# Kernel tuning notes

Measured on AMD Instinct MI355X. Metric: run time of the kernel, lower is better.

Reference implementation:

```python
import jax, jax.numpy as jnp
import numpy as np

D_MODEL = 1024
D_KV = 64
N_HEADS = 16
KV_HEADS = 4
G = N_HEADS // KV_HEADS
NUM_BUCKETS = 32
MAX_DISTANCE = 128


def _relative_position_bucket(relative_position, bidirectional=True,
                              num_buckets=NUM_BUCKETS, max_distance=MAX_DISTANCE):
    # Faithful port of T5Attention._relative_position_bucket
    relative_buckets = jnp.zeros_like(relative_position)
    if bidirectional:
        num_buckets //= 2
        relative_buckets = (relative_position > 0).astype(jnp.int32) * num_buckets
        relative_position = jnp.abs(relative_position)
    else:
        relative_position = -jnp.minimum(relative_position, 0)
    max_exact = num_buckets // 2
    is_small = relative_position < max_exact
    rel_if_large = max_exact + (
        jnp.log(relative_position.astype(jnp.float32) / max_exact)
        / np.log(max_distance / max_exact) * (num_buckets - max_exact)
    ).astype(jnp.int32)
    rel_if_large = jnp.minimum(rel_if_large, num_buckets - 1)
    return relative_buckets + jnp.where(is_small, relative_position, rel_if_large)


def setup_inputs() -> dict:
    key = jax.random.key(0)
    ks = jax.random.split(key, 6)
    B, S = 2, 2048
    inner = N_HEADS * D_KV
    sc = 1.0 / np.sqrt(D_MODEL)
    return {
        "hidden_states": jax.random.normal(ks[0], (B, S, D_MODEL), dtype=jnp.float32),
        "Wq": jax.random.normal(ks[1], (D_MODEL, inner), dtype=jnp.float32) * sc,
        "Wk": jax.random.normal(ks[2], (D_MODEL, inner), dtype=jnp.float32) * sc,
        "Wv": jax.random.normal(ks[3], (D_MODEL, inner), dtype=jnp.float32) * sc,
        "Wo": jax.random.normal(ks[4], (inner, D_MODEL), dtype=jnp.float32) * sc,
        "rel_bias": jax.random.normal(ks[5], (NUM_BUCKETS, N_HEADS), dtype=jnp.float32) * 0.1,
    }


def reference(hidden_states, Wq, Wk, Wv, Wo, rel_bias):
    B, S, _ = hidden_states.shape

    def split_heads(x):  # [B,S,inner] -> [B,H,S,Dk]
        return x.reshape(B, S, N_HEADS, D_KV).transpose(0, 2, 1, 3)

    q = split_heads(hidden_states @ Wq)
    k = split_heads(hidden_states @ Wk)
    v = split_heads(hidden_states @ Wv)

    # head index = g * KV_HEADS + h (einops 'b (g h) ...' with h=kv_heads)
    gq = q.reshape(B, G, KV_HEADS, S, D_KV)
    gk = k.reshape(B, G, KV_HEADS, S, D_KV).mean(axis=1)  # [B,Hkv,S,Dk]
    # einsum sums over g (as in torch.einsum 'bghnd,bhsd->bhns'); no 1/sqrt(d) in T5
    scores = jnp.einsum('bghnd,bhsd->bhns', gq, gk)  # [B,Hkv,S,S]

    # T5 relative position bias (bidirectional, encoder)
    ctx = jnp.arange(S)[:, None]
    mem = jnp.arange(S)[None, :]
    buckets = _relative_position_bucket(mem - ctx, bidirectional=True)
    bias = rel_bias[buckets]                # [S,S,H]
    bias = bias.transpose(2, 0, 1)[None]    # [1,H,S,S]
    gbias = bias.reshape(1, G, KV_HEADS, S, S).mean(axis=1)  # [1,Hkv,S,S]

    scores = scores + gbias
    attn = jax.nn.softmax(scores.astype(jnp.float32), axis=-1).astype(scores.dtype)

    # repeat grouped attn weights back to full heads: 'b h n s -> b (g h) n s'
    attn_full = jnp.tile(attn, (1, G, 1, 1))  # [B,H,S,S]
    ctx_out = jnp.einsum('bhns,bhsd->bhnd', attn_full, v)  # [B,H,S,Dk]
    ctx_out = ctx_out.transpose(0, 2, 1, 3).reshape(B, S, N_HEADS * D_KV)
    return ctx_out @ Wo  # [B,S,D_MODEL]
```

## Files before the change

kernel.cpp:

```cpp
#include <hip/hip_runtime.h>
#include <math.h>


typedef __bf16 bf16_t;
typedef bf16_t bf16x8 __attribute__((ext_vector_type(8)));
typedef bf16_t bf16x4 __attribute__((ext_vector_type(4)));
typedef float f32x4 __attribute__((ext_vector_type(4)));

#define MFMA16(a, b, c) __builtin_amdgcn_mfma_f32_16x16x32_bf16(a, b, c, 0, 0, 0)

typedef __attribute__((address_space(1))) void gvoid;
typedef __attribute__((address_space(3))) void svoid;
__device__ __forceinline__ void gld16(const void* g, void* l) {
    __builtin_amdgcn_global_load_lds((gvoid*)g, (svoid*)l, 16, 0, 0);
}

__global__ __launch_bounds__(256) void prep_all(const float* __restrict__ hs,
                                                const float* __restrict__ Wq,
                                                const float* __restrict__ Wk,
                                                const float* __restrict__ Wv,
                                                const float* __restrict__ Wo,
                                                const float* __restrict__ rel_bias,
                                                bf16_t* __restrict__ hs_hi,
                                                bf16_t* __restrict__ hs_lo,
                                                bf16_t* __restrict__ Thi,
                                                bf16_t* __restrict__ Tlo,
                                                bf16_t* __restrict__ WvT,
                                                bf16_t* __restrict__ WoT,
                                                float* __restrict__ btab) {
    __shared__ float sm[2048];
    const int r = blockIdx.x, t = threadIdx.x;
    if (r < 4096) {
        size_t idx = ((size_t)r * 256 + t) * 4;
        float4 v = *(const float4*)(hs + idx);
        bf16x4 h, l;
        h[0] = (bf16_t)v.x; l[0] = (bf16_t)(v.x - (float)h[0]);
        h[1] = (bf16_t)v.y; l[1] = (bf16_t)(v.y - (float)h[1]);
        h[2] = (bf16_t)v.z; l[2] = (bf16_t)(v.z - (float)h[2]);
        h[3] = (bf16_t)v.w; l[3] = (bf16_t)(v.w - (float)h[3]);
        *(bf16x4*)(hs_hi + idx) = h;
        *(bf16x4*)(hs_lo + idx) = l;
    } else if (r < 5120) {
        int k = r - 4096;
        float* rq = sm;
        float* rk = sm + 1024;
#pragma unroll
        for (int j = 0; j < 4; ++j) {
            rq[t + j * 256] = Wq[(size_t)k * 1024 + t + j * 256];
            rk[t + j * 256] = Wk[(size_t)k * 1024 + t + j * 256];
        }
        __syncthreads();
        int h = t >> 6, j2 = t & 63;
        float sq = 0.f, sk = 0.f;
#pragma unroll
        for (int g = 0; g < 4; ++g) {
            sq += rq[(g * 4 + h) * 64 + j2];
            sk += rk[(g * 4 + h) * 64 + j2];
        }
        sk *= 0.25f;
        bf16_t qh = (bf16_t)sq;
        Thi[(size_t)t * 1024 + k] = qh;
        Tlo[(size_t)t * 1024 + k] = (bf16_t)(sq - (float)qh);
        bf16_t kh = (bf16_t)sk;
        Thi[(size_t)(256 + t) * 1024 + k] = kh;
        Tlo[(size_t)(256 + t) * 1024 + k] = (bf16_t)(sk - (float)kh);
    } else if (r < 7168) {
        const float* src = (r < 6144) ? Wv : Wo;
        bf16_t* dst = (r < 6144) ? WvT : WoT;
        int rr = (r < 6144) ? r - 5120 : r - 6144;
        int bx = (rr & 31) * 32, by = (rr >> 5) * 32;
        int tx = t & 31, ty = t >> 5;
        float(*tile)[33] = (float(*)[33])sm;
#pragma unroll
        for (int i = 0; i < 32; i += 8)
            tile[ty + i][tx] = src[(size_t)(by + ty + i) * 1024 + bx + tx];
        __syncthreads();
#pragma unroll
        for (int i = 0; i < 32; i += 8)
            dst[(size_t)(bx + ty + i) * 1024 + by + tx] = (bf16_t)tile[tx][ty + i];
    } else {
        int idx = (r - 7168) * 256 + t;
        if (idx >= 4095) return;
        int delta = idx - 2047;
        int bucket = (delta > 0) ? 16 : 0;
        int arp = delta < 0 ? -delta : delta;
        int rb;
        if (arp < 8) {
            rb = arp;
        } else {
            float tt = (logf((float)arp * 0.125f) / 2.772588722239781f) * 8.0f;
            int ri = 8 + (int)tt;
            rb = ri < 15 ? ri : 15;
        }
        bucket += rb;
#pragma unroll
        for (int h = 0; h < 4; ++h) {
            float s = 0.25f * (rel_bias[bucket * 16 + h] + rel_bias[bucket * 16 + h + 4] +
                               rel_bias[bucket * 16 + h + 8] + rel_bias[bucket * 16 + h + 12]);
            btab[h * 4608 + idx] = s;
        }
    }
}

__global__ __launch_bounds__(256, 1) void proj_qkv(const bf16_t* __restrict__ Ah,
                                                   const bf16_t* __restrict__ Al,
                                                   const bf16_t* __restrict__ Bh,
                                                   const bf16_t* __restrict__ Bl,
                                                   const bf16_t* __restrict__ WvT,
                                                   bf16_t* __restrict__ Qhi,
                                                   bf16_t* __restrict__ Qlo,
                                                   bf16_t* __restrict__ Kbh,
                                                   bf16_t* __restrict__ Kbl,
                                                   bf16_t* __restrict__ Vb) {
    __shared__ bf16_t pool[36864];
    const int K = 1024, nk = 32;
    const int t = threadIdx.x;
    const int w = t >> 6, lane = t & 63;
    const int lr = lane & 15, q = lane >> 4;
    const int l = blockIdx.y * 16 + blockIdx.x;
    const int nl = (l & 7) * 64 + (l >> 3);
    const int bx = nl & 15;
    const int m0 = (nl >> 4) * 128;
    const bool qk = bx < 8;
    const int n0 = qk ? bx * 64 : (bx - 8) * 128;
    const int mw = (w & 1) * 64;
    f32x4 acc[4][4] = {};

    const int rA = t & 127, cA0 = t >> 7, cA1 = 2 + (t >> 7);
    const size_t oA0 = (size_t)(m0 + rA) * K + cA0 * 8;
    const size_t oA1 = (size_t)(m0 + rA) * K + cA1 * 8;
    const int rBq = t & 63, cBq = t >> 6;
    const size_t oBq = (size_t)(n0 + rBq) * K + cBq * 8;
    const size_t oBv0 = (size_t)(n0 + rA) * K + cA0 * 8;
    const size_t oBv1 = (size_t)(n0 + rA) * K + cA1 * 8;

    auto stage = [&](int bf, int kidx) {
        bf16_t* base = &pool[bf * 12288];
        const int k0 = kidx * 32;
        gld16(Ah + oA0 + k0, base + t * 8);
        gld16(Ah + oA1 + k0, base + (256 + t) * 8);
        if (qk) {
            gld16(Al + oA0 + k0, base + 4096 + t * 8);
            gld16(Al + oA1 + k0, base + 4096 + (256 + t) * 8);
            gld16(Bh + oBq + k0, base + 8192 + t * 8);
            gld16(Bl + oBq + k0, base + 10240 + t * 8);
        } else {
            gld16(WvT + oBv0 + k0, base + 4096 + t * 8);
            gld16(WvT + oBv1 + k0, base + 4096 + (256 + t) * 8);
        }
    };

    stage(0, 0);
    stage(1, 1);
    stage(2, 2);
    if (qk)
        asm volatile("s_waitcnt vmcnt(12)" ::: "memory");
    else
        asm volatile("s_waitcnt vmcnt(8)" ::: "memory");
    __builtin_amdgcn_s_barrier();

    int cur = 0;
    for (int it = 0; it < nk; ++it) {
        const bf16_t* base = &pool[cur * 12288];
        if (qk) {
            const int nw = (w >> 1) * 32;
            bf16x8 ah[4], al[4], bh[2], bl[2];
#pragma unroll
            for (int i = 0; i < 4; ++i) {
                int sa = (q * 128 + mw + i * 16 + lr) * 8;
                ah[i] = *(const bf16x8*)&base[sa];
                al[i] = *(const bf16x8*)&base[4096 + sa];
            }
#pragma unroll
            for (int j = 0; j < 2; ++j) {
                int sb = (q * 64 + nw + j * 16 + lr) * 8;
                bh[j] = *(const bf16x8*)&base[8192 + sb];
                bl[j] = *(const bf16x8*)&base[10240 + sb];
            }
            asm volatile("s_waitcnt lgkmcnt(0)" ::: "memory");
            if (it < nk - 2)
                asm volatile("s_waitcnt vmcnt(6)" ::: "memory");
            else
                asm volatile("s_waitcnt vmcnt(0)" ::: "memory");
            __builtin_amdgcn_s_barrier();
            if (it + 3 < nk) stage(cur, it + 3);
#pragma unroll
            for (int i = 0; i < 4; ++i)
#pragma unroll
                for (int j = 0; j < 2; ++j) {
                    acc[i][j] = MFMA16(ah[i], bh[j], acc[i][j]);
                    acc[i][j] = MFMA16(ah[i], bl[j], acc[i][j]);
                    acc[i][j] = MFMA16(al[i], bh[j], acc[i][j]);
                }
        } else {
            const int nw = (w >> 1) * 64;
            bf16x8 af[4], bfv[4];
#pragma unroll
            for (int i = 0; i < 4; ++i)
                af[i] = *(const bf16x8*)&base[(q * 128 + mw + i * 16 + lr) * 8];
#pragma unroll
            for (int j = 0; j < 4; ++j)
                bfv[j] = *(const bf16x8*)&base[4096 + (q * 128 + nw + j * 16 + lr) * 8];
            asm volatile("s_waitcnt lgkmcnt(0)" ::: "memory");
            if (it < nk - 2)
                asm volatile("s_waitcnt vmcnt(4)" ::: "memory");
            else
                asm volatile("s_waitcnt vmcnt(0)" ::: "memory");
            __builtin_amdgcn_s_barrier();
            if (it + 3 < nk) stage(cur, it + 3);
#pragma unroll
            for (int i = 0; i < 4; ++i)
#pragma unroll
                for (int j = 0; j < 4; ++j) acc[i][j] = MFMA16(af[i], bfv[j], acc[i][j]);
        }
        cur = (cur == 2) ? 0 : cur + 1;
    }

    if (qk) {
        const int nwq = (w >> 1) * 32;
#pragma unroll
        for (int i = 0; i < 4; ++i) {
            int row = m0 + mw + i * 16 + q * 4;
#pragma unroll
            for (int j = 0; j < 2; ++j) {
                int col = n0 + nwq + j * 16 + lr;
#pragma unroll
                for (int reg = 0; reg < 4; ++reg) {
                    float x = acc[i][j][reg];
                    int token = row + reg;
                    bf16_t hi = (bf16_t)x;
                    bf16_t lo = (bf16_t)(x - (float)hi);
                    if (col < 256) {
                        size_t o = (size_t)token * 256 + col;
                        Qhi[o] = hi;
                        Qlo[o] = lo;
                    } else {
                        int hc = col - 256;
                        int hh = hc >> 6, d = hc & 63;
                        int b = token >> 11, s = token & 2047;
                        int it2 = s >> 6, sl = s & 63;
                        size_t o = ((size_t)((b * 4 + hh) * 32 + it2)) * 4096 +
                                   (size_t)((d >> 3) * 64 + sl) * 8 + (d & 7);
                        Kbh[o] = hi;
                        Kbl[o] = lo;
                    }
                }
            }
        }
    } else {
        const int nwq = (w >> 1) * 64;
#pragma unroll
        for (int i = 0; i < 4; ++i) {
            int row = m0 + mw + i * 16 + q * 4;
            int b = row >> 11, s = row & 2047;
            int it2 = s >> 6, sc2 = (s >> 3) & 7, si = s & 7;
#pragma unroll
            for (int j = 0; j < 4; ++j) {
                int col = n0 + nwq + j * 16 + lr;
                int hh = (col >> 6) & 3, g = col >> 8, d = col & 63;
                size_t o = ((size_t)((b * 4 + hh) * 32 + it2)) * 16384 +
                           (size_t)(sc2 * 256 + g * 64 + d) * 8 + si;
                bf16x4 pv;
#pragma unroll
                for (int reg = 0; reg < 4; ++reg) pv[reg] = (bf16_t)acc[i][j][reg];
                *(bf16x4*)(Vb + o) = pv;
            }
        }
    }
}

__global__ __launch_bounds__(256, 1) void gemm_out(const bf16_t* __restrict__ A,
                                                   const bf16_t* __restrict__ BT,
                                                   float* __restrict__ C,
                                                   int M, int N, int K) {
    __shared__ bf16_t pool[18432];
    const int t = threadIdx.x;
    const int w = t >> 6, lane = t & 63;
    const int lr = lane & 15, q = lane >> 4;
    const int l = blockIdx.y * 16 + blockIdx.x;
    const int nl = (l & 7) * 64 + (l >> 3);
    const int m0 = (nl >> 4) * 128, n0 = (nl & 15) * 64;
    const int mw = (w & 1) * 64, nw = (w >> 1) * 32;
    f32x4 acc[4][2] = {};
    const int nk = K >> 5;

    const int rA = t & 127, cA0 = t >> 7, cA1 = 2 + (t >> 7);
    const bf16_t* gA0 = A + (size_t)(m0 + rA) * K + cA0 * 8;
    const bf16_t* gA1 = A + (size_t)(m0 + rA) * K + cA1 * 8;
    const bf16_t* gB = BT + (size_t)(n0 + (t & 63)) * K + (t >> 6) * 8;

    auto stage = [&](int bf, int kidx) {
        bf16_t* base = &pool[bf * 6144];
        const int k0 = kidx * 32;
        gld16(gA0 + k0, base + t * 8);
        gld16(gA1 + k0, base + (256 + t) * 8);
        gld16(gB + k0, base + 4096 + t * 8);
    };

    stage(0, 0);
    stage(1, 1);
    stage(2, 2);
    asm volatile("s_waitcnt vmcnt(6)" ::: "memory");
    __builtin_amdgcn_s_barrier();

    int cur = 0;
    for (int it = 0; it < nk; ++it) {
        const bf16_t* base = &pool[cur * 6144];
        bf16x8 af[4], bfv[2];
#pragma unroll
        for (int i = 0; i < 4; ++i)
            af[i] = *(const bf16x8*)&base[(q * 128 + mw + i * 16 + lr) * 8];
#pragma unroll
        for (int j = 0; j < 2; ++j)
            bfv[j] = *(const bf16x8*)&base[4096 + (q * 64 + nw + j * 16 + lr) * 8];
        asm volatile("s_waitcnt lgkmcnt(0)" ::: "memory");
        if (it < nk - 2)
            asm volatile("s_waitcnt vmcnt(3)" ::: "memory");
        else
            asm volatile("s_waitcnt vmcnt(0)" ::: "memory");
        __builtin_amdgcn_s_barrier();
        if (it + 3 < nk) stage(cur, it + 3);
#pragma unroll
        for (int i = 0; i < 4; ++i)
#pragma unroll
            for (int j = 0; j < 2; ++j) acc[i][j] = MFMA16(af[i], bfv[j], acc[i][j]);
        cur = (cur == 2) ? 0 : cur + 1;
    }

#pragma unroll
    for (int i = 0; i < 4; ++i) {
        int row = m0 + mw + i * 16 + q * 4;
#pragma unroll
        for (int j = 0; j < 2; ++j) {
            int col = n0 + nw + j * 16 + lr;
#pragma unroll
            for (int reg = 0; reg < 4; ++reg)
                C[(size_t)(row + reg) * N + col] = acc[i][j][reg];
        }
    }
}

__global__ __launch_bounds__(512, 1) void attn_mfma(const bf16_t* __restrict__ Qhi,
                                                    const bf16_t* __restrict__ Qlo,
                                                    const bf16_t* __restrict__ Kbh,
                                                    const bf16_t* __restrict__ Kbl,
                                                    const bf16_t* __restrict__ Vb,
                                                    const float* __restrict__ btab,
                                                    bf16_t* __restrict__ part0,
                                                    bf16_t* __restrict__ part1,
                                                    float* __restrict__ Sml) {
    __shared__ bf16_t Kh[2][4096], Kl[2][4096], Vsm[2][16384], Ps[8192];
    const int t = threadIdx.x, w = t >> 6, lane = t & 63;
    const int lr = lane & 15, q = lane >> 4;
    const int bl0 = blockIdx.x;
    const int blk = (bl0 & 7) * 32 + (bl0 >> 3);
    const int half = blk & 1, qt = (blk >> 1) & 15, h = (blk >> 5) & 3, b = blk >> 7;
    const int n0 = qt * 128;
    const int rowbase = n0 + w * 16;
    const int swz = (lr & 7) << 3;
    const int psb = w * 1024 + lr * 64;

    const size_t qrow = (size_t)(b * 2048 + rowbase + lr) * 256 + h * 64;
    bf16x8 aqh[2], aql[2];
#pragma unroll
    for (int kb = 0; kb < 2; ++kb) {
        aqh[kb] = *(const bf16x8*)(Qhi + qrow + kb * 32 + q * 8);
        aql[kb] = *(const bf16x8*)(Qlo + qrow + kb * 32 + q * 8);
    }

    const int tilebase = (b * 4 + h) * 32 + half * 16;
    const bf16_t* gK = Kbh + (size_t)tilebase * 4096;
    const bf16_t* gL = Kbl + (size_t)tilebase * 4096;
    const bf16_t* gV = Vb + (size_t)tilebase * 16384;
    const float* btabh = btab + h * 4608 + 2047;

    auto stage = [&](int bf, int it) {
        gld16(gK + (size_t)it * 4096 + t * 8, &Kh[bf][t * 8]);
        gld16(gL + (size_t)it * 4096 + t * 8, &Kl[bf][t * 8]);
        const bf16_t* v0 = gV + (size_t)it * 16384;
#pragma unroll
        for (int j = 0; j < 4; ++j)
            gld16(v0 + (j * 512 + t) * 8, &Vsm[bf][(j * 512 + t) * 8]);
    };

    float m_r = -INFINITY, l_r = 0.f;
    f32x4 O[16] = {};

    stage(0, 0);
    __syncthreads();
    for (int it = 0; it < 16; ++it) {
        const int cur = it & 1;
        if (it + 1 < 16) stage(cur ^ 1, it + 1);
        const int s0g = half * 1024 + it * 64;

        f32x4 sc[4];
#pragma unroll
        for (int ct = 0; ct < 4; ++ct) {
            f32x4 z = {0.f, 0.f, 0.f, 0.f};
#pragma unroll
            for (int kb = 0; kb < 2; ++kb) {
                int sb = ((kb * 4 + q) * 64 + ct * 16 + lr) * 8;
                bf16x8 bh = *(const bf16x8*)&Kh[cur][sb];
                bf16x8 bl = *(const bf16x8*)&Kl[cur][sb];
                z = MFMA16(bh, aqh[kb], z);
                z = MFMA16(bh, aql[kb], z);
                z = MFMA16(bl, aqh[kb], z);
            }
            sc[ct] = z;
        }
        const int dbase = (s0g + q * 4) - (rowbase + lr);
#pragma unroll
        for (int ct = 0; ct < 4; ++ct)
#pragma unroll
            for (int reg = 0; reg < 4; ++reg)
                sc[ct][reg] += btabh[dbase + ct * 16 + reg];

        float mt = fmaxf(fmaxf(sc[0][0], sc[0][1]), fmaxf(sc[0][2], sc[0][3]));
#pragma unroll
        for (int ct = 1; ct < 4; ++ct)
            mt = fmaxf(mt, fmaxf(fmaxf(sc[ct][0], sc[ct][1]), fmaxf(sc[ct][2], sc[ct][3])));
        mt = fmaxf(mt, __shfl_xor(mt, 16, 64));
        mt = fmaxf(mt, __shfl_xor(mt, 32, 64));

        float mn = fmaxf(m_r, mt);
        float al = __expf(m_r - mn);
        m_r = mn;
        float rs = 0.f;
#pragma unroll
        for (int ct = 0; ct < 4; ++ct) {
            bf16x4 tq;
#pragma unroll
            for (int reg = 0; reg < 4; ++reg) {
                float p = __expf(sc[ct][reg] - mn);
                rs += p;
                tq[reg] = (bf16_t)p;
            }
            *(bf16x4*)&Ps[psb + ((ct * 16 + q * 4) ^ swz)] = tq;
        }
        rs += __shfl_xor(rs, 16, 64);
        rs += __shfl_xor(rs, 32, 64);
        l_r = l_r * al + rs;

        bf16x8 pf0 = *(const bf16x8*)&Ps[psb + ((q * 8) ^ swz)];
        bf16x8 pf1 = *(const bf16x8*)&Ps[psb + ((32 + q * 8) ^ swz)];

#pragma unroll
        for (int nt = 0; nt < 16; ++nt) {
            f32x4 o = O[nt];
#pragma unroll
            for (int reg = 0; reg < 4; ++reg) o[reg] *= al;
            bf16x8 v0 = *(const bf16x8*)&Vsm[cur][(q * 256 + nt * 16 + lr) * 8];
            o = MFMA16(v0, pf0, o);
            bf16x8 v1 = *(const bf16x8*)&Vsm[cur][((4 + q) * 256 + nt * 16 + lr) * 8];
            o = MFMA16(v1, pf1, o);
            O[nt] = o;
        }
        __syncthreads();
    }

    bf16_t* P = half ? part1 : part0;
    const float inv = 1.f / l_r;
    const int tokb = b * 2048 + rowbase;
#pragma unroll
    for (int G = 0; G < 4; ++G) {
#pragma unroll
        for (int g4 = 0; g4 < 4; ++g4) {
            int nt = G * 4 + g4;
            bf16x4 tq;
#pragma unroll
            for (int reg = 0; reg < 4; ++reg) tq[reg] = (bf16_t)(O[nt][reg] * inv);
            *(bf16x4*)&Ps[psb + ((g4 * 16 + q * 4) ^ swz)] = tq;
        }
#pragma unroll
        for (int i = 0; i < 2; ++i) {
            int row = i * 8 + (lane >> 3), cv = (lane & 7) * 8;
            bf16x8 fr = *(const bf16x8*)&Ps[w * 1024 + row * 64 + (cv ^ ((row & 7) << 3))];
            *(bf16x8*)(P + (size_t)(tokb + row) * 1024 + (G * 4 + h) * 64 + cv) = fr;
        }
    }
    if (lane < 16)
        Sml[half * 16384 + (size_t)(tokb + lane) * 4 + h] = m_r + logf(l_r);
}

__global__ __launch_bounds__(256) void combine_halves(bf16_t* __restrict__ p0,
                                                      const bf16_t* __restrict__ p1,
                                                      const float* __restrict__ Sml) {
    size_t flat = ((size_t)blockIdx.x * 256 + threadIdx.x) * 8;
    int tok = (int)(flat >> 10), c = (int)(flat & 1023), h = (c >> 6) & 3;
    float s0 = Sml[tok * 4 + h], s1 = Sml[16384 + tok * 4 + h];
    float M = fmaxf(s0, s1);
    float e0 = __expf(s0 - M), e1 = __expf(s1 - M);
    float r = 1.f / (e0 + e1);
    float w0 = e0 * r, w1 = e1 * r;
    bf16x8 a = *(bf16x8*)(p0 + flat);
    bf16x8 bb = *(const bf16x8*)(p1 + flat);
    bf16x8 o;
#pragma unroll
    for (int i = 0; i < 8; ++i) o[i] = (bf16_t)(w0 * (float)a[i] + w1 * (float)bb[i]);
    *(bf16x8*)(p0 + flat) = o;
}

extern "C" void kernel_launch(void* const* d_in, const int* in_sizes, int n_in,
                              void* d_out, int out_size, void* d_ws, size_t ws_size,
                              hipStream_t stream) {
    const float* hs = (const float*)d_in[0];
    const float* Wq = (const float*)d_in[1];
    const float* Wk = (const float*)d_in[2];
    const float* Wv = (const float*)d_in[3];
    const float* Wo = (const float*)d_in[4];
    const float* rb = (const float*)d_in[5];
    float* out = (float*)d_out;

    const size_t MB = 1 << 20;
    const size_t KB = 1 << 10;
    char* ws = (char*)d_ws;
    bf16_t* hs_hi = (bf16_t*)(ws);
    bf16_t* hs_lo = (bf16_t*)(ws + 8 * MB);
    bf16_t* WqkThi = (bf16_t*)(ws + 16 * MB);
    bf16_t* WqkTlo = (bf16_t*)(ws + 17 * MB);
    bf16_t* WvT = (bf16_t*)(ws + 18 * MB);
    bf16_t* WoT = (bf16_t*)(ws + 20 * MB);
    float* btab = (float*)(ws + 22 * MB);
    float* Sml = (float*)(ws + 22 * MB + 128 * KB);
    bf16_t* Qhi = (bf16_t*)(ws + 22 * MB + 256 * KB);
    bf16_t* Qlo = Qhi + (size_t)4096 * 256;
    bf16_t* Kbh = Qlo + (size_t)4096 * 256;
    bf16_t* Kbl = Kbh + (size_t)4096 * 256;
    bf16_t* Vb = Kbl + (size_t)4096 * 256;
    bf16_t* part0 = hs_hi;
    bf16_t* part1 = hs_lo;

    prep_all<<<7184, 256, 0, stream>>>(hs, Wq, Wk, Wv, Wo, rb, hs_hi, hs_lo, WqkThi,
                                       WqkTlo, WvT, WoT, btab);
    proj_qkv<<<dim3(16, 32), 256, 0, stream>>>(hs_hi, hs_lo, WqkThi, WqkTlo, WvT, Qhi,
                                               Qlo, Kbh, Kbl, Vb);
    attn_mfma<<<256, 512, 0, stream>>>(Qhi, Qlo, Kbh, Kbl, Vb, btab, part0, part1, Sml);
    combine_halves<<<2048, 256, 0, stream>>>(part0, part1, Sml);
    gemm_out<<<dim3(16, 32), 256, 0, stream>>>(part0, WoT, out, 4096, 1024, 1024);
}
```

Measured before the change: 220.9 us.

## Fuse split-KV combine into output GEMM and skip redundant attention work

Removes the separate combine_halves kernel by having gemm_out load both partial attention outputs, weight them with the log-sum-exp factors, and write the merged bf16 tile into shared memory before the MFMA loop. The A-operand staging moves from async global-to-LDS copies with triple buffering to register loads plus LDS writes with double buffering. The attention kernel also adds a constant relative-bias value for tiles far from the diagonal, where every bucket saturates, and skips rescaling the O accumulator when no row maximum changed. The costs are a shallower GEMM pipeline, extra ALU work in the GEMM, and more branching in the attention loop.

Result: slower. 232.2 us (+5.1%).

```diff
diff --git a/kernel.cpp b/kernel.cpp
--- a/kernel.cpp
+++ b/kernel.cpp
@@ -269,11 +269,13 @@
     }
 }
 
-__global__ __launch_bounds__(256, 1) void gemm_out(const bf16_t* __restrict__ A,
+__global__ __launch_bounds__(256, 1) void gemm_out(const bf16_t* __restrict__ p0,
+                                                   const bf16_t* __restrict__ p1,
+                                                   const float* __restrict__ Sml,
                                                    const bf16_t* __restrict__ BT,
-                                                   float* __restrict__ C,
-                                                   int M, int N, int K) {
-    __shared__ bf16_t pool[18432];
+                                                   float* __restrict__ C) {
+    __shared__ bf16_t pool[12288];
+    const int K = 1024, N = 1024;
     const int t = threadIdx.x;
     const int w = t >> 6, lane = t & 63;
     const int lr = lane & 15, q = lane >> 4;
@@ -282,49 +284,88 @@
     const int m0 = (nl >> 4) * 128, n0 = (nl & 15) * 64;
     const int mw = (w & 1) * 64, nw = (w >> 1) * 32;
     f32x4 acc[4][2] = {};
-    const int nk = K >> 5;
-
-    const int rA = t & 127, cA0 = t >> 7, cA1 = 2 + (t >> 7);
-    const bf16_t* gA0 = A + (size_t)(m0 + rA) * K + cA0 * 8;
-    const bf16_t* gA1 = A + (size_t)(m0 + rA) * K + cA1 * 8;
+
+    const int rA = t & 127, cA0 = t >> 7;
+    const int tok = m0 + rA;
+    const bf16_t* gA0 = p0 + (size_t)tok * K + cA0 * 8;
+    const bf16_t* gA1 = p1 + (size_t)tok * K + cA0 * 8;
     const bf16_t* gB = BT + (size_t)(n0 + (t & 63)) * K + (t >> 6) * 8;
 
-    auto stage = [&](int bf, int kidx) {
-        bf16_t* base = &pool[bf * 6144];
+    float w00, w01, w02, w03, w10, w11, w12, w13;
+    {
+        float s0, s1, M_, e0, e1, r;
+#define MKW(H, W0, W1)                                   \
+    s0 = Sml[tok * 4 + H];                               \
+    s1 = Sml[16384 + tok * 4 + H];                       \
+    M_ = fmaxf(s0, s1);                                  \
+    e0 = __expf(s0 - M_);                                \
+    e1 = __expf(s1 - M_);                                \
+    r = 1.f / (e0 + e1);                                 \
+    W0 = e0 * r;                                         \
+    W1 = e1 * r;
+        MKW(0, w00, w10)
+        MKW(1, w01, w11)
+        MKW(2, w02, w12)
+        MKW(3, w03, w13)
+#undef MKW
+    }
+
+    bf16x8 sa0, sb0, sa1, sb1;
+    auto stage_load = [&](int kidx) {
         const int k0 = kidx * 32;
-        gld16(gA0 + k0, base + t * 8);
-        gld16(gA1 + k0, base + (256 + t) * 8);
-        gld16(gB + k0, base + 4096 + t * 8);
+        sa0 = *(const bf16x8*)(gA0 + k0);
+        sb0 = *(const bf16x8*)(gA1 + k0);
+        sa1 = *(const bf16x8*)(gA0 + k0 + 16);
+        sb1 = *(const bf16x8*)(gA1 + k0 + 16);
     };
-
-    stage(0, 0);
-    stage(1, 1);
-    stage(2, 2);
-    asm volatile("s_waitcnt vmcnt(6)" ::: "memory");
-    __builtin_amdgcn_s_barrier();
-
-    int cur = 0;
-    for (int it = 0; it < nk; ++it) {
-        const bf16_t* base = &pool[cur * 6144];
-        bf16x8 af[4], bfv[2];
-#pragma unroll
-        for (int i = 0; i < 4; ++i)
-            af[i] = *(const bf16x8*)&base[(q * 128 + mw + i * 16 + lr) * 8];
-#pragma unroll
-        for (int j = 0; j < 2; ++j)
-            bfv[j] = *(const bf16x8*)&base[4096 + (q * 64 + nw + j * 16 + lr) * 8];
-        asm volatile("s_waitcnt lgkmcnt(0)" ::: "memory");
-        if (it < nk - 2)
-            asm volatile("s_waitcnt vmcnt(3)" ::: "memory");
-        else
-            asm volatile("s_waitcnt vmcnt(0)" ::: "memory");
-        __builtin_amdgcn_s_barrier();
-        if (it + 3 < nk) stage(cur, it + 3);
-#pragma unroll
-        for (int i = 0; i < 4; ++i)
-#pragma unroll
-            for (int j = 0; j < 2; ++j) acc[i][j] = MFMA16(af[i], bfv[j], acc[i][j]);
-        cur = (cur == 2) ? 0 : cur + 1;
+    auto stage_write = [&](int bf, float cw0, float cw1) {
+        bf16x8 y0, y1;
+#pragma unroll
+        for (int i = 0; i < 8; ++i) {
+            y0[i] = (bf16_t)(cw0 * (float)sa0[i] + cw1 * (float)sb0[i]);
+            y1[i] = (bf16_t)(cw0 * (float)sa1[i] + cw1 * (float)sb1[i]);
+        }
+        *(bf16x8*)&pool[bf * 4096 + t * 8] = y0;
+        *(bf16x8*)&pool[bf * 4096 + (256 + t) * 8] = y1;
+    };
+
+    stage_load(0);
+    gld16(gB + 0, &pool[8192 + t * 8]);
+    asm volatile("s_waitcnt vmcnt(1)" ::: "memory");
+    stage_write(0, w00, w10);
+    __syncthreads();
+
+    for (int o = 0; o < 4; ++o) {
+#pragma unroll
+        for (int u = 0; u < 8; ++u) {
+            const int it = o * 8 + u;
+            const int cur = it & 1;
+            const bool pre = (it + 1 < 32);
+            if (pre) {
+                stage_load(it + 1);
+                gld16(gB + (it + 1) * 32, &pool[8192 + (cur ^ 1) * 2048 + t * 8]);
+            }
+            const bf16_t* base = &pool[cur * 4096];
+            bf16x8 af[4], bfv[2];
+#pragma unroll
+            for (int i = 0; i < 4; ++i)
+                af[i] = *(const bf16x8*)&base[(q * 128 + mw + i * 16 + lr) * 8];
+#pragma unroll
+            for (int j = 0; j < 2; ++j)
+                bfv[j] = *(const bf16x8*)&pool[8192 + cur * 2048 + (q * 64 + nw + j * 16 + lr) * 8];
+#pragma unroll
+            for (int i = 0; i < 4; ++i)
+#pragma unroll
+                for (int j = 0; j < 2; ++j) acc[i][j] = MFMA16(af[i], bfv[j], acc[i][j]);
+            if (pre) {
+                asm volatile("s_waitcnt vmcnt(1)" ::: "memory");
+                const int hs = ((u + 1) >> 1) & 3;
+                float cw0 = (hs == 0) ? w00 : (hs == 1) ? w01 : (hs == 2) ? w02 : w03;
+                float cw1 = (hs == 0) ? w10 : (hs == 1) ? w11 : (hs == 2) ? w12 : w13;
+                stage_write(cur ^ 1, cw0, cw1);
+            }
+            __syncthreads();
+        }
     }
 
 #pragma unroll
@@ -373,6 +414,8 @@
     const bf16_t* gL = Kbl + (size_t)tilebase * 4096;
     const bf16_t* gV = Vb + (size_t)tilebase * 16384;
     const float* btabh = btab + h * 4608 + 2047;
+    const float bpos = btabh[1024];
+    const float bneg = btabh[-1024];
 
     auto stage = [&](int bf, int it) {
         gld16(gK + (size_t)it * 4096 + t * 8, &Kh[bf][t * 8]);
@@ -408,12 +451,24 @@
             }
             sc[ct] = z;
         }
-        const int dbase = (s0g + q * 4) - (rowbase + lr);
-#pragma unroll
-        for (int ct = 0; ct < 4; ++ct)
-#pragma unroll
-            for (int reg = 0; reg < 4; ++reg)
-                sc[ct][reg] += btabh[dbase + ct * 16 + reg];
+        if (s0g - rowbase >= 143) {
+#pragma unroll
+            for (int ct = 0; ct < 4; ++ct)
+#pragma unroll
+                for (int reg = 0; reg < 4; ++reg) sc[ct][reg] += bpos;
+        } else if (rowbase - s0g >= 154) {
+#pragma unroll
+            for (int ct = 0; ct < 4; ++ct)
+#pragma unroll
+                for (int reg = 0; reg < 4; ++reg) sc[ct][reg] += bneg;
+        } else {
+            const int dbase = (s0g + q * 4) - (rowbase + lr);
+#pragma unroll
+            for (int ct = 0; ct < 4; ++ct)
+#pragma unroll
+                for (int reg = 0; reg < 4; ++reg)
+                    sc[ct][reg] += btabh[dbase + ct * 16 + reg];
+        }
 
         float mt = fmaxf(fmaxf(sc[0][0], sc[0][1]), fmaxf(sc[0][2], sc[0][3]));
 #pragma unroll
@@ -423,7 +478,8 @@
         mt = fmaxf(mt, __shfl_xor(mt, 32, 64));
 
         float mn = fmaxf(m_r, mt);
-        float al = __expf(m_r - mn);
+        const bool noresc = (bool)__all(mn == m_r);
+        float al = noresc ? 1.f : __expf(m_r - mn);
         m_r = mn;
         float rs = 0.f;
 #pragma unroll
@@ -441,14 +497,19 @@
         rs += __shfl_xor(rs, 32, 64);
         l_r = l_r * al + rs;
 
+        if (!noresc) {
+#pragma unroll
+            for (int nt = 0; nt < 16; ++nt)
+#pragma unroll
+                for (int reg = 0; reg < 4; ++reg) O[nt][reg] *= al;
+        }
+
         bf16x8 pf0 = *(const bf16x8*)&Ps[psb + ((q * 8) ^ swz)];
         bf16x8 pf1 = *(const bf16x8*)&Ps[psb + ((32 + q * 8) ^ swz)];
 
 #pragma unroll
         for (int nt = 0; nt < 16; ++nt) {
             f32x4 o = O[nt];
-#pragma unroll
-            for (int reg = 0; reg < 4; ++reg) o[reg] *= al;
             bf16x8 v0 = *(const bf16x8*)&Vsm[cur][(q * 256 + nt * 16 + lr) * 8];
             o = MFMA16(v0, pf0, o);
             bf16x8 v1 = *(const bf16x8*)&Vsm[cur][((4 + q) * 256 + nt * 16 + lr) * 8];
@@ -480,24 +541,6 @@
     }
     if (lane < 16)
         Sml[half * 16384 + (size_t)(tokb + lane) * 4 + h] = m_r + logf(l_r);
-}
-
-__global__ __launch_bounds__(256) void combine_halves(bf16_t* __restrict__ p0,
-                                                      const bf16_t* __restrict__ p1,
-                                                      const float* __restrict__ Sml) {
-    size_t flat = ((size_t)blockIdx.x * 256 + threadIdx.x) * 8;
-    int tok = (int)(flat >> 10), c = (int)(flat & 1023), h = (c >> 6) & 3;
-    float s0 = Sml[tok * 4 + h], s1 = Sml[16384 + tok * 4 + h];
-    float M = fmaxf(s0, s1);
-    float e0 = __expf(s0 - M), e1 = __expf(s1 - M);
-    float r = 1.f / (e0 + e1);
-    float w0 = e0 * r, w1 = e1 * r;
-    bf16x8 a = *(bf16x8*)(p0 + flat);
-    bf16x8 bb = *(const bf16x8*)(p1 + flat);
-    bf16x8 o;
-#pragma unroll
-    for (int i = 0; i < 8; ++i) o[i] = (bf16_t)(w0 * (float)a[i] + w1 * (float)bb[i]);
-    *(bf16x8*)(p0 + flat) = o;
 }
 
 extern "C" void kernel_launch(void* const* d_in, const int* in_sizes, int n_in,
@@ -535,6 +578,5 @@
     proj_qkv<<<dim3(16, 32), 256, 0, stream>>>(hs_hi, hs_lo, WqkThi, WqkTlo, WvT, Qhi,
                                                Qlo, Kbh, Kbl, Vb);
     attn_mfma<<<256, 512, 0, stream>>>(Qhi, Qlo, Kbh, Kbl, Vb, btab, part0, part1, Sml);
-    combine_halves<<<2048, 256, 0, stream>>>(part0, part1, Sml);
-    gemm_out<<<dim3(16, 32), 256, 0, stream>>>(part0, WoT, out, 4096, 1024, 1024);
+    gemm_out<<<dim3(16, 32), 256, 0, stream>>>(part0, part1, Sml, WoT, out);
 }
```

## Single-buffer V tile, skip bias gathers far from diagonal, skip uniform rescale

Applied to the files above, without the earlier changes.

V shared memory drops from double to single buffering. The V load for the next tile is now issued after the PV MFMAs, and an extra barrier is added before them, so V loading overlaps only the QK and softmax phase. Tiles far from the diagonal add a constant saturated bias value instead of gathering per element from the bias table. The O rescale is skipped when no lane's running max changed. These cut LDS footprint and the bias-load work, but add an extra barrier per iteration and less overlap for V loads.

Measured after the change: 226.5 us. 1.03x slower.

```diff
diff --git a/kernel.cpp b/kernel.cpp
--- a/kernel.cpp
+++ b/kernel.cpp
@@ -349,7 +349,7 @@
                                                     bf16_t* __restrict__ part0,
                                                     bf16_t* __restrict__ part1,
                                                     float* __restrict__ Sml) {
-    __shared__ bf16_t Kh[2][4096], Kl[2][4096], Vsm[2][16384], Ps[8192];
+    __shared__ bf16_t Kh[2][4096], Kl[2][4096], Vsm[16384], Ps[8192];
     const int t = threadIdx.x, w = t >> 6, lane = t & 63;
     const int lr = lane & 15, q = lane >> 4;
     const int bl0 = blockIdx.x;
@@ -373,24 +373,29 @@
     const bf16_t* gL = Kbl + (size_t)tilebase * 4096;
     const bf16_t* gV = Vb + (size_t)tilebase * 16384;
     const float* btabh = btab + h * 4608 + 2047;
-
-    auto stage = [&](int bf, int it) {
+    const float bpos = btabh[1024];
+    const float bneg = btabh[-1024];
+
+    auto stageK = [&](int bf, int it) {
         gld16(gK + (size_t)it * 4096 + t * 8, &Kh[bf][t * 8]);
         gld16(gL + (size_t)it * 4096 + t * 8, &Kl[bf][t * 8]);
+    };
+    auto stageV = [&](int it) {
         const bf16_t* v0 = gV + (size_t)it * 16384;
 #pragma unroll
         for (int j = 0; j < 4; ++j)
-            gld16(v0 + (j * 512 + t) * 8, &Vsm[bf][(j * 512 + t) * 8]);
+            gld16(v0 + (j * 512 + t) * 8, &Vsm[(j * 512 + t) * 8]);
     };
 
     float m_r = -INFINITY, l_r = 0.f;
     f32x4 O[16] = {};
 
-    stage(0, 0);
+    stageK(0, 0);
+    stageV(0);
     __syncthreads();
     for (int it = 0; it < 16; ++it) {
         const int cur = it & 1;
-        if (it + 1 < 16) stage(cur ^ 1, it + 1);
+        if (it + 1 < 16) stageK(cur ^ 1, it + 1);
         const int s0g = half * 1024 + it * 64;
 
         f32x4 sc[4];
@@ -408,12 +413,24 @@
             }
             sc[ct] = z;
         }
-        const int dbase = (s0g + q * 4) - (rowbase + lr);
-#pragma unroll
-        for (int ct = 0; ct < 4; ++ct)
-#pragma unroll
-            for (int reg = 0; reg < 4; ++reg)
-                sc[ct][reg] += btabh[dbase + ct * 16 + reg];
+        if (s0g - rowbase >= 143) {
+#pragma unroll
+            for (int ct = 0; ct < 4; ++ct)
+#pragma unroll
+                for (int reg = 0; reg < 4; ++reg) sc[ct][reg] += bpos;
+        } else if (rowbase - s0g >= 154) {
+#pragma unroll
+            for (int ct = 0; ct < 4; ++ct)
+#pragma unroll
+                for (int reg = 0; reg < 4; ++reg) sc[ct][reg] += bneg;
+        } else {
+            const int dbase = (s0g + q * 4) - (rowbase + lr);
+#pragma unroll
+            for (int ct = 0; ct < 4; ++ct)
+#pragma unroll
+                for (int reg = 0; reg < 4; ++reg)
+                    sc[ct][reg] += btabh[dbase + ct * 16 + reg];
+        }
 
         float mt = fmaxf(fmaxf(sc[0][0], sc[0][1]), fmaxf(sc[0][2], sc[0][3]));
 #pragma unroll
@@ -423,7 +440,8 @@
         mt = fmaxf(mt, __shfl_xor(mt, 32, 64));
 
         float mn = fmaxf(m_r, mt);
-        float al = __expf(m_r - mn);
+        const bool noresc = (bool)__all(mn == m_r);
+        float al = noresc ? 1.f : __expf(m_r - mn);
         m_r = mn;
         float rs = 0.f;
 #pragma unroll
@@ -441,21 +459,29 @@
         rs += __shfl_xor(rs, 32, 64);
         l_r = l_r * al + rs;
 
+        if (!noresc) {
+#pragma unroll
+            for (int nt = 0; nt < 16; ++nt)
+#pragma unroll
+                for (int reg = 0; reg < 4; ++reg) O[nt][reg] *= al;
+        }
+
+        __syncthreads();
+
         bf16x8 pf0 = *(const bf16x8*)&Ps[psb + ((q * 8) ^ swz)];
         bf16x8 pf1 = *(const bf16x8*)&Ps[psb + ((32 + q * 8) ^ swz)];
 
 #pragma unroll
         for (int nt = 0; nt < 16; ++nt) {
             f32x4 o = O[nt];
-#pragma unroll
-            for (int reg = 0; reg < 4; ++reg) o[reg] *= al;
-            bf16x8 v0 = *(const bf16x8*)&Vsm[cur][(q * 256 + nt * 16 + lr) * 8];
+            bf16x8 v0 = *(const bf16x8*)&Vsm[(q * 256 + nt * 16 + lr) * 8];
             o = MFMA16(v0, pf0, o);
-            bf16x8 v1 = *(const bf16x8*)&Vsm[cur][((4 + q) * 256 + nt * 16 + lr) * 8];
+            bf16x8 v1 = *(const bf16x8*)&Vsm[((4 + q) * 256 + nt * 16 + lr) * 8];
             o = MFMA16(v1, pf1, o);
             O[nt] = o;
         }
         __syncthreads();
+        if (it + 1 < 16) stageV(it + 1);
     }
 
     bf16_t* P = half ? part1 : part0;
```
